# Kernel optimization log

Hardware: AMD Instinct MI355X
Metric: run time of the kernel (lower is better)

The kernel has to match this reference:

```python
import jax, jax.numpy as jnp
import numpy as np

N_GRIDS = 64          # n_grids
FEATS = 2             # feats_per_grid
DIM = 64              # feat_grid_dim (D=H=W)
N_PTS = 1 << 19       # query points per batch
N_NEURONS = 64        # tcnn FullyFusedMLP n_neurons


def setup_inputs() -> dict:
    key = jax.random.key(0)
    ks = jax.random.split(key, 8)
    x = jax.random.uniform(ks[0], (N_PTS, 3), jnp.float32, -1.0, 1.0)
    r = jax.random.normal(ks[1], (N_GRIDS, 4), jnp.float32)                      # quaternions
    s = 1.0 + 0.05 * jax.random.normal(ks[2], (N_GRIDS, 3), jnp.float32)         # scales ~1
    t = 0.1 * jax.random.normal(ks[3], (N_GRIDS, 3), jnp.float32)                # translations
    features = 0.1 * jax.random.normal(ks[4], (N_GRIDS, FEATS, DIM, DIM, DIM), jnp.float32)
    d_in = N_GRIDS * FEATS
    W0 = jax.random.normal(ks[5], (N_NEURONS, d_in), jnp.float32) / np.sqrt(d_in)
    W1 = jax.random.normal(ks[6], (N_NEURONS, N_NEURONS), jnp.float32) / np.sqrt(N_NEURONS)
    W2 = jax.random.normal(ks[7], (1, N_NEURONS), jnp.float32) / np.sqrt(N_NEURONS)
    return {"x": x, "r": r, "s": s, "t": t, "features": features,
            "W0": W0, "W1": W1, "W2": W2}


def quat_to_rot(q):
    # q: [G,4] (w,x,y,z); normalized rotation matrices [G,3,3]
    q = q / jnp.linalg.norm(q, axis=-1, keepdims=True)
    w, x, y, z = q[:, 0], q[:, 1], q[:, 2], q[:, 3]
    R = jnp.stack([
        1 - 2 * (y * y + z * z), 2 * (x * y - w * z),     2 * (x * z + w * y),
        2 * (x * y + w * z),     1 - 2 * (x * x + z * z), 2 * (y * z - w * x),
        2 * (x * z - w * y),     2 * (y * z + w * x),     1 - 2 * (x * x + y * y),
    ], axis=-1)
    return R.reshape(-1, 3, 3)


def trilinear_sample(features, pts):
    # features: [G,C,D,H,W]; pts: [G,N,3] in [-1,1], (x,y,z) -> (W,H,D) axes,
    # align_corners=True, zero padding (torch grid_sample semantics).
    G, C, D, H, W = features.shape
    gx = (pts[..., 0] + 1.0) * 0.5 * (W - 1)
    gy = (pts[..., 1] + 1.0) * 0.5 * (H - 1)
    gz = (pts[..., 2] + 1.0) * 0.5 * (D - 1)
    x0f, y0f, z0f = jnp.floor(gx), jnp.floor(gy), jnp.floor(gz)
    fx, fy, fz = gx - x0f, gy - y0f, gz - z0f
    x0, y0, z0 = x0f.astype(jnp.int32), y0f.astype(jnp.int32), z0f.astype(jnp.int32)
    x1, y1, z1 = x0 + 1, y0 + 1, z0 + 1
    feat_flat = features.reshape(G, C, D * H * W)

    def corner(xi, yi, zi, w):
        valid = ((xi >= 0) & (xi < W) & (yi >= 0) & (yi < H) & (zi >= 0) & (zi < D))
        xc = jnp.clip(xi, 0, W - 1)
        yc = jnp.clip(yi, 0, H - 1)
        zc = jnp.clip(zi, 0, D - 1)
        idx = (zc * H + yc) * W + xc                       # [G,N]
        v = jnp.take_along_axis(feat_flat, idx[:, None, :], axis=2)  # [G,C,N]
        return v * (w * valid)[:, None, :]

    out = (corner(x0, y0, z0, (1 - fx) * (1 - fy) * (1 - fz))
         + corner(x1, y0, z0, fx * (1 - fy) * (1 - fz))
         + corner(x0, y1, z0, (1 - fx) * fy * (1 - fz))
         + corner(x1, y1, z0, fx * fy * (1 - fz))
         + corner(x0, y0, z1, (1 - fx) * (1 - fy) * fz)
         + corner(x1, y0, z1, fx * (1 - fy) * fz)
         + corner(x0, y1, z1, (1 - fx) * fy * fz)
         + corner(x1, y1, z1, fx * fy * fz))
    return out  # [G,C,N]


def encode(x, r, s, t, features):
    R = quat_to_rot(r)                                     # [G,3,3]
    # per-grid affine: p' = (R p) * s + t  -> [G,N,3]
    tp = jnp.einsum('gij,nj->gni', R, x) * s[:, None, :] + t[:, None, :]
    sampled = trilinear_sample(features, tp)               # [G,C,N]
    N = x.shape[0]
    return jnp.transpose(sampled, (2, 0, 1)).reshape(N, -1)  # [N, G*C]


def reference(x, r, s, t, features, W0, W1, W2):
    feats = encode(x, r, s, t, features)                   # [N, 128]
    h = jax.nn.relu(feats @ W0.T)                          # [N, 64]
    h = jax.nn.relu(h @ W1.T)                              # [N, 64]
    return h @ W2.T                                        # [N, 1]
```

## Files before the change

### kernel.cpp

```cpp
#include <hip/hip_runtime.h>
#include <hip/hip_fp16.h>

#define NG    64
#define NC    2
#define DIMG  64
#define NPTS  (1u << 19)
#define NN    64
#define DIN   (NG * NC)
#define VOX   (DIMG * DIMG * DIMG)
#define CELLS 16
#define NCELL (CELLS * CELLS * CELLS)

typedef _Float16 f16;
typedef _Float16 f16x8 __attribute__((ext_vector_type(8)));
typedef float    f32x4 __attribute__((ext_vector_type(4)));

#define OFF_M      0
#define OFF_W0F    768
#define OFF_W1F    4864
#define OFF_HIST   6912
#define OFF_CNT    11008
#define OFF_SORT   15104
#define OFF_FEATP  2112256
#define WS_REQ_BYTES (((size_t)OFF_FEATP + 2ull * NG * VOX) * 4 + 64)

__device__ __forceinline__ f16x8 as_f16x8(uint4 u) {
    union { uint4 u; f16x8 h; } c; c.u = u; return c.h;
}
__device__ __forceinline__ float2 h2f(uint u) {
    union { uint u; __half2 h; } c; c.u = u; return __half22float2(c.h);
}

__global__ void prep_kernel(const float* __restrict__ r, const float* __restrict__ s,
                            const float* __restrict__ t, const float* __restrict__ W0,
                            const float* __restrict__ W1, float* __restrict__ ws) {
    int tid = blockIdx.x * blockDim.x + threadIdx.x;
    int nth = gridDim.x * blockDim.x;
    float* M  = ws + OFF_M;
    f16* W0f  = (f16*)(ws + OFF_W0F);
    f16* W1f  = (f16*)(ws + OFF_W1F);
    if (tid < NG) {
        float qw = r[tid*4+0], qx = r[tid*4+1], qy = r[tid*4+2], qz = r[tid*4+3];
        float inv = 1.0f / sqrtf(qw*qw + qx*qx + qy*qy + qz*qz);
        qw *= inv; qx *= inv; qy *= inv; qz *= inv;
        float R0 = 1.f - 2.f*(qy*qy + qz*qz), R1 = 2.f*(qx*qy - qw*qz), R2 = 2.f*(qx*qz + qw*qy);
        float R3 = 2.f*(qx*qy + qw*qz), R4 = 1.f - 2.f*(qx*qx + qz*qz), R5 = 2.f*(qy*qz - qw*qx);
        float R6 = 2.f*(qx*qz - qw*qy), R7 = 2.f*(qy*qz + qw*qx), R8 = 1.f - 2.f*(qx*qx + qy*qy);
        float s0 = s[tid*3+0], s1 = s[tid*3+1], s2 = s[tid*3+2];
        M[tid*12+ 0] = s0*R0; M[tid*12+ 1] = s0*R1; M[tid*12+ 2] = s0*R2; M[tid*12+ 3] = t[tid*3+0];
        M[tid*12+ 4] = s1*R3; M[tid*12+ 5] = s1*R4; M[tid*12+ 6] = s1*R5; M[tid*12+ 7] = t[tid*3+1];
        M[tid*12+ 8] = s2*R6; M[tid*12+ 9] = s2*R7; M[tid*12+10] = s2*R8; M[tid*12+11] = t[tid*3+2];
    }
    for (int idx = tid; idx < 4*4*64*8; idx += nth) {
        int tn = idx >> 11, kc = (idx >> 9) & 3, lane = (idx >> 3) & 63, j = idx & 7;
        int n = tn*16 + (lane & 15);
        int k = kc*32 + (lane >> 4)*8 + j;
        W0f[idx] = (f16)W0[n*DIN + k];
    }
    for (int idx = tid; idx < 4*2*64*8; idx += nth) {
        int tn = idx >> 10, kc2 = (idx >> 9) & 1, lane = (idx >> 3) & 63, j = idx & 7;
        int n = tn*16 + (lane & 15);
        int k = kc2*32 + (lane >> 4)*8 + j;
        W1f[idx] = (f16)W1[n*NN + k];
    }
}

__global__ __launch_bounds__(256) void repack_pairs(const float* __restrict__ feat,
                                                    uint4* __restrict__ featP4) {
    size_t i = (size_t)blockIdx.x * 256 + threadIdx.x;
    size_t g = i / (VOX/4), vq = i % (VOX/4);
    const float* b0 = feat + g * (size_t)(NC * VOX);
    const float* b1 = b0 + VOX;
    float4 a = ((const float4*)b0)[vq];
    float4 b = ((const float4*)b1)[vq];
    int vnext = (int)vq * 4 + 4; if (vnext > VOX - 1) vnext = VOX - 1;
    float a4 = b0[vnext], b4 = b1[vnext];
    __half2 h0 = __floats2half2_rn(a.x, b.x);
    __half2 h1 = __floats2half2_rn(a.y, b.y);
    __half2 h2 = __floats2half2_rn(a.z, b.z);
    __half2 h3 = __floats2half2_rn(a.w, b.w);
    __half2 h4 = __floats2half2_rn(a4, b4);
    union { uint4 u[2]; __half2 h[8]; } o;
    o.h[0] = h0; o.h[1] = h1;
    o.h[2] = h1; o.h[3] = h2;
    o.h[4] = h2; o.h[5] = h3;
    o.h[6] = h3; o.h[7] = h4;
    featP4[i*2 + 0] = o.u[0];
    featP4[i*2 + 1] = o.u[1];
}

__device__ __forceinline__ int cell_of(float px, float py, float pz) {
    int ix = (int)((px + 1.f) * (0.5f * CELLS)); ix = ix < 0 ? 0 : (ix > CELLS-1 ? CELLS-1 : ix);
    int iy = (int)((py + 1.f) * (0.5f * CELLS)); iy = iy < 0 ? 0 : (iy > CELLS-1 ? CELLS-1 : iy);
    int iz = (int)((pz + 1.f) * (0.5f * CELLS)); iz = iz < 0 ? 0 : (iz > CELLS-1 ? CELLS-1 : iz);
    return (iz * CELLS + iy) * CELLS + ix;
}

__global__ __launch_bounds__(256) void count_kernel(const float* __restrict__ xs,
                                                    unsigned* __restrict__ hist) {
    unsigned pt = blockIdx.x * blockDim.x + threadIdx.x;
    atomicAdd(&hist[cell_of(xs[pt*3+0], xs[pt*3+1], xs[pt*3+2])], 1u);
}

__global__ __launch_bounds__(256) void scan_kernel(const unsigned* __restrict__ hist,
                                                   unsigned* __restrict__ cnt) {
    __shared__ unsigned part[256];
    int t = threadIdx.x;
    unsigned base = t * (NCELL / 256);
    unsigned loc[NCELL / 256];
    unsigned sum = 0;
#pragma unroll
    for (int i = 0; i < NCELL / 256; ++i) { loc[i] = sum; sum += hist[base + i]; }
    part[t] = sum;
    __syncthreads();
    for (int off = 1; off < 256; off <<= 1) {
        unsigned v = (t >= off) ? part[t - off] : 0u;
        __syncthreads();
        part[t] += v;
        __syncthreads();
    }
    unsigned prev = (t == 0) ? 0u : part[t - 1];
#pragma unroll
    for (int i = 0; i < NCELL / 256; ++i) cnt[base + i] = prev + loc[i];
}

__global__ __launch_bounds__(256) void scatter_kernel(const float* __restrict__ xs,
                                                      unsigned* __restrict__ cnt,
                                                      float4* __restrict__ sorted) {
    unsigned pt = blockIdx.x * blockDim.x + threadIdx.x;
    float px = xs[pt*3+0], py = xs[pt*3+1], pz = xs[pt*3+2];
    unsigned pos = atomicAdd(&cnt[cell_of(px, py, pz)], 1u);
    sorted[pos] = make_float4(px, py, pz, __int_as_float((int)pt));
}

__global__ __launch_bounds__(256, 4) void amgsrn_fused(
        const float4* __restrict__ sorted, const uint2* __restrict__ featP,
        const float* __restrict__ ws, const float* __restrict__ W2,
        float* __restrict__ out) {
    __shared__ uint4 SH[2048];
    __shared__ float SOUT[256];
    const float* M = ws + OFF_M;
    const f16x8* W0f = (const f16x8*)(ws + OFF_W0F);
    const f16x8* W1f = (const f16x8*)(ws + OFF_W1F);

    int t = threadIdx.x;
    int lane = t & 63, w = t >> 6;
    int tmw = t >> 4, mrow = t & 15;

    float4 p4 = sorted[blockIdx.x * 256u + t];
    float px = p4.x, py = p4.y, pz = p4.z;
    int orig = __float_as_int(p4.w);

    f32x4 acc[4][4];
#pragma unroll
    for (int a = 0; a < 4; ++a)
#pragma unroll
        for (int b = 0; b < 4; ++b) acc[a][b] = (f32x4){0.f, 0.f, 0.f, 0.f};

    for (int kc = 0; kc < 4; ++kc) {
        uint4* buf = &SH[(kc & 1) * 1024];
#pragma unroll
        for (int c = 0; c < 4; ++c) {
            uint pk[4];
#pragma unroll
            for (int gi = 0; gi < 4; ++gi) {
                int g = kc * 16 + c * 4 + gi;
                const float* m = M + g * 12;
                float tx = m[0]*px + m[1]*py + m[2]*pz + m[3];
                float ty = m[4]*px + m[5]*py + m[6]*pz + m[7];
                float tz = m[8]*px + m[9]*py + m[10]*pz + m[11];
                float gx = (tx + 1.f) * (0.5f * (DIMG - 1));
                float gy = (ty + 1.f) * (0.5f * (DIMG - 1));
                float gz = (tz + 1.f) * (0.5f * (DIMG - 1));
                float f0 = 0.f, f1 = 0.f;
                if (gx > -1.f && gx < (float)DIMG && gy > -1.f && gy < (float)DIMG &&
                    gz > -1.f && gz < (float)DIMG) {
                    float x0f = floorf(gx), y0f = floorf(gy), z0f = floorf(gz);
                    float fx = gx - x0f, fy = gy - y0f, fz = gz - z0f;
                    int x0 = (int)x0f, y0 = (int)y0f, z0 = (int)z0f;
                    int x1 = x0 + 1, y1 = y0 + 1, z1 = z0 + 1;
                    float wx0 = (x0 >= 0)      ? (1.f - fx) : 0.f;
                    float wx1 = (x1 <= DIMG-1) ? fx         : 0.f;
                    float wy0 = (y0 >= 0)      ? (1.f - fy) : 0.f;
                    float wy1 = (y1 <= DIMG-1) ? fy         : 0.f;
                    float wz0 = (z0 >= 0)      ? (1.f - fz) : 0.f;
                    float wz1 = (z1 <= DIMG-1) ? fz         : 0.f;
                    int cx0 = max(x0, 0), cx1 = min(x1, DIMG-1);
                    int cy0 = max(y0, 0), cy1 = min(y1, DIMG-1);
                    int cz0 = max(z0, 0), cz1 = min(z1, DIMG-1);
                    bool adj = (cx1 == cx0 + 1);

                    const uint2* P = featP + (size_t)g * VOX;
                    int r00 = (cz0 * DIMG + cy0) * DIMG + cx0;
                    int r01 = (cz0 * DIMG + cy1) * DIMG + cx0;
                    int r10 = (cz1 * DIMG + cy0) * DIMG + cx0;
                    int r11 = (cz1 * DIMG + cy1) * DIMG + cx0;
                    uint2 e00 = P[r00], e01 = P[r01], e10 = P[r10], e11 = P[r11];
                    float2 l00 = h2f(e00.x), u00 = h2f(adj ? e00.y : e00.x);
                    float2 l01 = h2f(e01.x), u01 = h2f(adj ? e01.y : e01.x);
                    float2 l10 = h2f(e10.x), u10 = h2f(adj ? e10.y : e10.x);
                    float2 l11 = h2f(e11.x), u11 = h2f(adj ? e11.y : e11.x);

                    float w00 = wz0*wy0, w01 = wz0*wy1, w10 = wz1*wy0, w11 = wz1*wy1;
                    f0 = w00*(wx0*l00.x + wx1*u00.x) + w01*(wx0*l01.x + wx1*u01.x)
                       + w10*(wx0*l10.x + wx1*u10.x) + w11*(wx0*l11.x + wx1*u11.x);
                    f1 = w00*(wx0*l00.y + wx1*u00.y) + w01*(wx0*l01.y + wx1*u01.y)
                       + w10*(wx0*l10.y + wx1*u10.y) + w11*(wx0*l11.y + wx1*u11.y);
                }
                union { uint u; __half2 h; } pkc;
                pkc.h = __floats2half2_rn(f0, f1);
                pk[gi] = pkc.u;
            }
            buf[tmw * 64 + c * 16 + mrow] = make_uint4(pk[0], pk[1], pk[2], pk[3]);
        }
        __syncthreads();
#pragma unroll
        for (int im = 0; im < 4; ++im) {
            f16x8 af = as_f16x8(buf[(w * 4 + im) * 64 + lane]);
#pragma unroll
            for (int tn = 0; tn < 4; ++tn) {
                f16x8 bf = W0f[(tn * 4 + kc) * 64 + lane];
                acc[im][tn] = __builtin_amdgcn_mfma_f32_16x16x32_f16(af, bf, acc[im][tn], 0, 0, 0);
            }
        }
    }
    __syncthreads();

    f16* Hh = (f16*)SH;
#pragma unroll
    for (int im = 0; im < 4; ++im) {
        int tm = w * 4 + im;
#pragma unroll
        for (int tn = 0; tn < 4; ++tn) {
            int n = tn * 16 + (lane & 15);
            int kc2 = n >> 5, koct = (n >> 3) & 3, j = n & 7;
#pragma unroll
            for (int r = 0; r < 4; ++r) {
                int mloc = (lane >> 4) * 4 + r;
                Hh[tm * 1024 + kc2 * 512 + (koct * 16 + mloc) * 8 + j] =
                    (f16)fmaxf(acc[im][tn][r], 0.f);
            }
        }
    }
    __syncthreads();

    f32x4 acc2[4][4];
#pragma unroll
    for (int a = 0; a < 4; ++a)
#pragma unroll
        for (int b = 0; b < 4; ++b) acc2[a][b] = (f32x4){0.f, 0.f, 0.f, 0.f};
#pragma unroll
    for (int kc2 = 0; kc2 < 2; ++kc2) {
#pragma unroll
        for (int im = 0; im < 4; ++im) {
            f16x8 af = as_f16x8(SH[(w * 4 + im) * 128 + kc2 * 64 + lane]);
#pragma unroll
            for (int tn = 0; tn < 4; ++tn) {
                f16x8 bf = W1f[(tn * 2 + kc2) * 64 + lane];
                acc2[im][tn] = __builtin_amdgcn_mfma_f32_16x16x32_f16(af, bf, acc2[im][tn], 0, 0, 0);
            }
        }
    }

    float w2v[4];
#pragma unroll
    for (int tn = 0; tn < 4; ++tn) w2v[tn] = W2[tn * 16 + (lane & 15)];
    __syncthreads();
#pragma unroll
    for (int im = 0; im < 4; ++im) {
#pragma unroll
        for (int r = 0; r < 4; ++r) {
            float pp = 0.f;
#pragma unroll
            for (int tn = 0; tn < 4; ++tn) pp += fmaxf(acc2[im][tn][r], 0.f) * w2v[tn];
            pp += __shfl_xor(pp, 1);
            pp += __shfl_xor(pp, 2);
            pp += __shfl_xor(pp, 4);
            pp += __shfl_xor(pp, 8);
            if ((lane & 15) == 0)
                SOUT[w * 64 + im * 16 + (lane >> 4) * 4 + r] = pp;
        }
    }
    __syncthreads();
    out[orig] = SOUT[t];
}

__global__ __launch_bounds__(256) void amgsrn_fallback(
        const float* __restrict__ xs, const float* __restrict__ feat,
        const float* __restrict__ ws, const float* __restrict__ W0,
        const float* __restrict__ W1, const float* __restrict__ W2,
        float* __restrict__ out) {
    const float* M = ws + OFF_M;
    unsigned pt = blockIdx.x * blockDim.x + threadIdx.x;
    float px = xs[pt*3+0], py = xs[pt*3+1], pz = xs[pt*3+2];
    float h0[NN];
#pragma unroll
    for (int j = 0; j < NN; ++j) h0[j] = 0.f;
    for (int g = 0; g < NG; ++g) {
        const float* m = M + g * 12;
        float tx = m[0]*px + m[1]*py + m[2]*pz + m[3];
        float ty = m[4]*px + m[5]*py + m[6]*pz + m[7];
        float tz = m[8]*px + m[9]*py + m[10]*pz + m[11];
        float gx = (tx + 1.f) * (0.5f * (DIMG - 1));
        float gy = (ty + 1.f) * (0.5f * (DIMG - 1));
        float gz = (tz + 1.f) * (0.5f * (DIMG - 1));
        float f0 = 0.f, f1 = 0.f;
        if (gx > -1.f && gx < (float)DIMG && gy > -1.f && gy < (float)DIMG &&
            gz > -1.f && gz < (float)DIMG) {
            float x0f = floorf(gx), y0f = floorf(gy), z0f = floorf(gz);
            float fx = gx - x0f, fy = gy - y0f, fz = gz - z0f;
            int x0 = (int)x0f, y0 = (int)y0f, z0 = (int)z0f;
            int x1 = x0 + 1, y1 = y0 + 1, z1 = z0 + 1;
            float wx0 = (x0 >= 0)      ? (1.f - fx) : 0.f;
            float wx1 = (x1 <= DIMG-1) ? fx         : 0.f;
            float wy0 = (y0 >= 0)      ? (1.f - fy) : 0.f;
            float wy1 = (y1 <= DIMG-1) ? fy         : 0.f;
            float wz0 = (z0 >= 0)      ? (1.f - fz) : 0.f;
            float wz1 = (z1 <= DIMG-1) ? fz         : 0.f;
            int cx0 = max(x0, 0), cx1 = min(x1, DIMG-1);
            int cy0 = max(y0, 0), cy1 = min(y1, DIMG-1);
            int cz0 = max(z0, 0), cz1 = min(z1, DIMG-1);
            const float* b0 = feat + (size_t)g * (NC * VOX);
            const float* b1 = b0 + VOX;
            int r00 = (cz0 * DIMG + cy0) * DIMG;
            int r01 = (cz0 * DIMG + cy1) * DIMG;
            int r10 = (cz1 * DIMG + cy0) * DIMG;
            int r11 = (cz1 * DIMG + cy1) * DIMG;
            f0 = wz0*(wy0*(wx0*b0[r00+cx0] + wx1*b0[r00+cx1]) + wy1*(wx0*b0[r01+cx0] + wx1*b0[r01+cx1]))
               + wz1*(wy0*(wx0*b0[r10+cx0] + wx1*b0[r10+cx1]) + wy1*(wx0*b0[r11+cx0] + wx1*b0[r11+cx1]));
            f1 = wz0*(wy0*(wx0*b1[r00+cx0] + wx1*b1[r00+cx1]) + wy1*(wx0*b1[r01+cx0] + wx1*b1[r01+cx1]))
               + wz1*(wy0*(wx0*b1[r10+cx0] + wx1*b1[r10+cx1]) + wy1*(wx0*b1[r11+cx0] + wx1*b1[r11+cx1]));
        }
#pragma unroll
        for (int j = 0; j < NN; ++j) {
            h0[j] = fmaf(f0, W0[j*DIN + g*2 + 0], h0[j]);
            h0[j] = fmaf(f1, W0[j*DIN + g*2 + 1], h0[j]);
        }
    }
#pragma unroll
    for (int j = 0; j < NN; ++j) h0[j] = fmaxf(h0[j], 0.f);
    float outv = 0.f;
    for (int j = 0; j < NN; ++j) {
        float acc = 0.f;
#pragma unroll
        for (int k = 0; k < NN; ++k) acc = fmaf(h0[k], W1[j*NN + k], acc);
        outv = fmaf(fmaxf(acc, 0.f), W2[j], outv);
    }
    out[pt] = outv;
}

extern "C" void kernel_launch(void* const* d_in, const int* in_sizes, int n_in,
                              void* d_out, int out_size, void* d_ws, size_t ws_size,
                              hipStream_t stream) {
    const float* x    = (const float*)d_in[0];
    const float* r    = (const float*)d_in[1];
    const float* s    = (const float*)d_in[2];
    const float* t    = (const float*)d_in[3];
    const float* feat = (const float*)d_in[4];
    const float* W0   = (const float*)d_in[5];
    const float* W1   = (const float*)d_in[6];
    const float* W2   = (const float*)d_in[7];
    float* outp = (float*)d_out;
    float* ws   = (float*)d_ws;

    prep_kernel<<<64, 256, 0, stream>>>(r, s, t, W0, W1, ws);

    if (ws_size >= WS_REQ_BYTES) {
        unsigned* hist   = (unsigned*)(ws + OFF_HIST);
        unsigned* cnt    = (unsigned*)(ws + OFF_CNT);
        float4*   sorted = (float4*)(ws + OFF_SORT);
        uint4*    featP4 = (uint4*)(ws + OFF_FEATP);

        hipMemsetAsync(hist, 0, NCELL * sizeof(unsigned), stream);
        repack_pairs<<<(NG * VOX / 4) / 256, 256, 0, stream>>>(feat, featP4);
        count_kernel<<<NPTS / 256, 256, 0, stream>>>(x, hist);
        scan_kernel<<<1, 256, 0, stream>>>(hist, cnt);
        scatter_kernel<<<NPTS / 256, 256, 0, stream>>>(x, cnt, sorted);
        amgsrn_fused<<<NPTS / 256, 256, 0, stream>>>(sorted, (const uint2*)featP4, ws, W2, outp);
    } else {
        amgsrn_fallback<<<NPTS / 256, 256, 0, stream>>>(x, feat, ws, W0, W1, W2, outp);
    }
}
```

Before: 466.6 us.

## Merge prep into repack, fuse count with scan, use packed fp16 x-lerp

Folds the weight conversion, histogram zeroing and affine-matrix setup into the feature repack kernel. It also merges the histogram count and prefix scan into one kernel, where the last block to finish does the scan. This removes a memset and two kernel launches with their serialization gaps. The trilinear x-interpolation now runs in packed fp16 vector math before widening to fp32, which saves ALU work but lowers interpolation precision.

```diff
diff --git a/kernel.cpp b/kernel.cpp
--- a/kernel.cpp
+++ b/kernel.cpp
@@ -12,7 +12,9 @@
 #define NCELL (CELLS * CELLS * CELLS)
 
 typedef _Float16 f16;
+typedef _Float16 f16x2 __attribute__((ext_vector_type(2)));
 typedef _Float16 f16x8 __attribute__((ext_vector_type(8)));
+typedef float    f32x2 __attribute__((ext_vector_type(2)));
 typedef float    f32x4 __attribute__((ext_vector_type(4)));
 
 #define OFF_M      0
@@ -20,54 +22,58 @@
 #define OFF_W1F    4864
 #define OFF_HIST   6912
 #define OFF_CNT    11008
-#define OFF_SORT   15104
-#define OFF_FEATP  2112256
+#define OFF_DONE   15104
+#define OFF_SORT   15168
+#define OFF_FEATP  2112320
 #define WS_REQ_BYTES (((size_t)OFF_FEATP + 2ull * NG * VOX) * 4 + 64)
 
 __device__ __forceinline__ f16x8 as_f16x8(uint4 u) {
     union { uint4 u; f16x8 h; } c; c.u = u; return c.h;
 }
-__device__ __forceinline__ float2 h2f(uint u) {
-    union { uint u; __half2 h; } c; c.u = u; return __half22float2(c.h);
-}
-
-__global__ void prep_kernel(const float* __restrict__ r, const float* __restrict__ s,
-                            const float* __restrict__ t, const float* __restrict__ W0,
-                            const float* __restrict__ W1, float* __restrict__ ws) {
-    int tid = blockIdx.x * blockDim.x + threadIdx.x;
-    int nth = gridDim.x * blockDim.x;
-    float* M  = ws + OFF_M;
-    f16* W0f  = (f16*)(ws + OFF_W0F);
-    f16* W1f  = (f16*)(ws + OFF_W1F);
-    if (tid < NG) {
-        float qw = r[tid*4+0], qx = r[tid*4+1], qy = r[tid*4+2], qz = r[tid*4+3];
+__device__ __forceinline__ f16x2 uas_h2(uint u) {
+    union { uint u; f16x2 h; } c; c.u = u; return c.h;
+}
+
+__global__ __launch_bounds__(256) void prep_repack(
+        const float* __restrict__ r, const float* __restrict__ s,
+        const float* __restrict__ t, const float* __restrict__ W0,
+        const float* __restrict__ W1, const float* __restrict__ feat,
+        float* __restrict__ ws) {
+    unsigned i = blockIdx.x * 256u + threadIdx.x;
+
+    if (i < 8192) {
+        f16* W0f = (f16*)(ws + OFF_W0F);
+        int tn = i >> 11, kc = (i >> 9) & 3, lane = (i >> 3) & 63, j = i & 7;
+        int n = tn*16 + (lane & 15);
+        int k = kc*32 + (lane >> 4)*8 + j;
+        W0f[i] = (f16)W0[n*DIN + k];
+    } else if (i < 12288) {
+        f16* W1f = (f16*)(ws + OFF_W1F);
+        int idx = i - 8192;
+        int tn = idx >> 10, kc2 = (idx >> 9) & 1, lane = (idx >> 3) & 63, j = idx & 7;
+        int n = tn*16 + (lane & 15);
+        int k = kc2*32 + (lane >> 4)*8 + j;
+        W1f[idx] = (f16)W1[n*NN + k];
+    } else if (i < 16384) {
+        ((unsigned*)(ws + OFF_HIST))[i - 12288] = 0u;
+    } else if (i == 16384) {
+        ((unsigned*)(ws + OFF_DONE))[0] = 0u;
+    } else if (i >= 16448 && i < 16448 + NG) {
+        int g = i - 16448;
+        float* M = ws + OFF_M;
+        float qw = r[g*4+0], qx = r[g*4+1], qy = r[g*4+2], qz = r[g*4+3];
         float inv = 1.0f / sqrtf(qw*qw + qx*qx + qy*qy + qz*qz);
         qw *= inv; qx *= inv; qy *= inv; qz *= inv;
         float R0 = 1.f - 2.f*(qy*qy + qz*qz), R1 = 2.f*(qx*qy - qw*qz), R2 = 2.f*(qx*qz + qw*qy);
         float R3 = 2.f*(qx*qy + qw*qz), R4 = 1.f - 2.f*(qx*qx + qz*qz), R5 = 2.f*(qy*qz - qw*qx);
         float R6 = 2.f*(qx*qz - qw*qy), R7 = 2.f*(qy*qz + qw*qx), R8 = 1.f - 2.f*(qx*qx + qy*qy);
-        float s0 = s[tid*3+0], s1 = s[tid*3+1], s2 = s[tid*3+2];
-        M[tid*12+ 0] = s0*R0; M[tid*12+ 1] = s0*R1; M[tid*12+ 2] = s0*R2; M[tid*12+ 3] = t[tid*3+0];
-        M[tid*12+ 4] = s1*R3; M[tid*12+ 5] = s1*R4; M[tid*12+ 6] = s1*R5; M[tid*12+ 7] = t[tid*3+1];
-        M[tid*12+ 8] = s2*R6; M[tid*12+ 9] = s2*R7; M[tid*12+10] = s2*R8; M[tid*12+11] = t[tid*3+2];
-    }
-    for (int idx = tid; idx < 4*4*64*8; idx += nth) {
-        int tn = idx >> 11, kc = (idx >> 9) & 3, lane = (idx >> 3) & 63, j = idx & 7;
-        int n = tn*16 + (lane & 15);
-        int k = kc*32 + (lane >> 4)*8 + j;
-        W0f[idx] = (f16)W0[n*DIN + k];
-    }
-    for (int idx = tid; idx < 4*2*64*8; idx += nth) {
-        int tn = idx >> 10, kc2 = (idx >> 9) & 1, lane = (idx >> 3) & 63, j = idx & 7;
-        int n = tn*16 + (lane & 15);
-        int k = kc2*32 + (lane >> 4)*8 + j;
-        W1f[idx] = (f16)W1[n*NN + k];
-    }
-}
-
-__global__ __launch_bounds__(256) void repack_pairs(const float* __restrict__ feat,
-                                                    uint4* __restrict__ featP4) {
-    size_t i = (size_t)blockIdx.x * 256 + threadIdx.x;
+        float s0 = s[g*3+0], s1 = s[g*3+1], s2 = s[g*3+2];
+        M[g*12+ 0] = s0*R0; M[g*12+ 1] = s0*R1; M[g*12+ 2] = s0*R2; M[g*12+ 3] = t[g*3+0];
+        M[g*12+ 4] = s1*R3; M[g*12+ 5] = s1*R4; M[g*12+ 6] = s1*R5; M[g*12+ 7] = t[g*3+1];
+        M[g*12+ 8] = s2*R6; M[g*12+ 9] = s2*R7; M[g*12+10] = s2*R8; M[g*12+11] = t[g*3+2];
+    }
+
+    uint4* featP4 = (uint4*)(ws + OFF_FEATP);
     size_t g = i / (VOX/4), vq = i % (VOX/4);
     const float* b0 = feat + g * (size_t)(NC * VOX);
     const float* b1 = b0 + VOX;
@@ -85,8 +91,8 @@
     o.h[2] = h1; o.h[3] = h2;
     o.h[4] = h2; o.h[5] = h3;
     o.h[6] = h3; o.h[7] = h4;
-    featP4[i*2 + 0] = o.u[0];
-    featP4[i*2 + 1] = o.u[1];
+    featP4[(size_t)i*2 + 0] = o.u[0];
+    featP4[(size_t)i*2 + 1] = o.u[1];
 }
 
 __device__ __forceinline__ int cell_of(float px, float py, float pz) {
@@ -96,38 +102,48 @@
     return (iz * CELLS + iy) * CELLS + ix;
 }
 
-__global__ __launch_bounds__(256) void count_kernel(const float* __restrict__ xs,
-                                                    unsigned* __restrict__ hist) {
-    unsigned pt = blockIdx.x * blockDim.x + threadIdx.x;
+__global__ __launch_bounds__(256) void count_scan(const float* __restrict__ xs,
+                                                  unsigned* __restrict__ hist,
+                                                  unsigned* __restrict__ cnt,
+                                                  unsigned* __restrict__ done) {
+    unsigned pt = blockIdx.x * 256u + threadIdx.x;
     atomicAdd(&hist[cell_of(xs[pt*3+0], xs[pt*3+1], xs[pt*3+2])], 1u);
-}
-
-__global__ __launch_bounds__(256) void scan_kernel(const unsigned* __restrict__ hist,
-                                                   unsigned* __restrict__ cnt) {
-    __shared__ unsigned part[256];
-    int t = threadIdx.x;
-    unsigned base = t * (NCELL / 256);
-    unsigned loc[NCELL / 256];
-    unsigned sum = 0;
-#pragma unroll
-    for (int i = 0; i < NCELL / 256; ++i) { loc[i] = sum; sum += hist[base + i]; }
-    part[t] = sum;
-    __syncthreads();
-    for (int off = 1; off < 256; off <<= 1) {
-        unsigned v = (t >= off) ? part[t - off] : 0u;
+    __threadfence();
+    __syncthreads();
+    __shared__ unsigned isLast;
+    if (threadIdx.x == 0)
+        isLast = (atomicAdd(done, 1u) == gridDim.x - 1) ? 1u : 0u;
+    __syncthreads();
+    if (isLast) {
+        __threadfence();
+        __shared__ unsigned part[256];
+        int t = threadIdx.x;
+        unsigned base = t * (NCELL / 256);
+        unsigned loc[NCELL / 256];
+        unsigned sum = 0;
+#pragma unroll
+        for (int k = 0; k < NCELL / 256; ++k) {
+            loc[k] = sum;
+            sum += atomicAdd(&hist[base + k], 0u);
+        }
+        part[t] = sum;
         __syncthreads();
-        part[t] += v;
-        __syncthreads();
-    }
-    unsigned prev = (t == 0) ? 0u : part[t - 1];
-#pragma unroll
-    for (int i = 0; i < NCELL / 256; ++i) cnt[base + i] = prev + loc[i];
+        for (int off = 1; off < 256; off <<= 1) {
+            unsigned v = (t >= off) ? part[t - off] : 0u;
+            __syncthreads();
+            part[t] += v;
+            __syncthreads();
+        }
+        unsigned prev = (t == 0) ? 0u : part[t - 1];
+#pragma unroll
+        for (int k = 0; k < NCELL / 256; ++k) cnt[base + k] = prev + loc[k];
+    }
 }
 
 __global__ __launch_bounds__(256) void scatter_kernel(const float* __restrict__ xs,
                                                       unsigned* __restrict__ cnt,
                                                       float4* __restrict__ sorted) {
-    unsigned pt = blockIdx.x * blockDim.x + threadIdx.x;
+    unsigned pt = blockIdx.x * 256u + threadIdx.x;
     float px = xs[pt*3+0], py = xs[pt*3+1], pz = xs[pt*3+2];
     unsigned pos = atomicAdd(&cnt[cell_of(px, py, pz)], 1u);
     sorted[pos] = make_float4(px, py, pz, __int_as_float((int)pt));
@@ -172,7 +188,7 @@
                 float gx = (tx + 1.f) * (0.5f * (DIMG - 1));
                 float gy = (ty + 1.f) * (0.5f * (DIMG - 1));
                 float gz = (tz + 1.f) * (0.5f * (DIMG - 1));
-                float f0 = 0.f, f1 = 0.f;
+                f32x2 fv = (f32x2){0.f, 0.f};
                 if (gx > -1.f && gx < (float)DIMG && gy > -1.f && gy < (float)DIMG &&
                     gz > -1.f && gz < (float)DIMG) {
                     float x0f = floorf(gx), y0f = floorf(gy), z0f = floorf(gz);
@@ -196,19 +212,19 @@
                     int r10 = (cz1 * DIMG + cy0) * DIMG + cx0;
                     int r11 = (cz1 * DIMG + cy1) * DIMG + cx0;
                     uint2 e00 = P[r00], e01 = P[r01], e10 = P[r10], e11 = P[r11];
-                    float2 l00 = h2f(e00.x), u00 = h2f(adj ? e00.y : e00.x);
-                    float2 l01 = h2f(e01.x), u01 = h2f(adj ? e01.y : e01.x);
-                    float2 l10 = h2f(e10.x), u10 = h2f(adj ? e10.y : e10.x);
-                    float2 l11 = h2f(e11.x), u11 = h2f(adj ? e11.y : e11.x);
-
+                    f16 hwx0 = (f16)wx0, hwx1 = (f16)wx1;
+                    f16x2 rx00 = uas_h2(e00.x)*hwx0 + uas_h2(adj ? e00.y : e00.x)*hwx1;
+                    f16x2 rx01 = uas_h2(e01.x)*hwx0 + uas_h2(adj ? e01.y : e01.x)*hwx1;
+                    f16x2 rx10 = uas_h2(e10.x)*hwx0 + uas_h2(adj ? e10.y : e10.x)*hwx1;
+                    f16x2 rx11 = uas_h2(e11.x)*hwx0 + uas_h2(adj ? e11.y : e11.x)*hwx1;
                     float w00 = wz0*wy0, w01 = wz0*wy1, w10 = wz1*wy0, w11 = wz1*wy1;
-                    f0 = w00*(wx0*l00.x + wx1*u00.x) + w01*(wx0*l01.x + wx1*u01.x)
-                       + w10*(wx0*l10.x + wx1*u10.x) + w11*(wx0*l11.x + wx1*u11.x);
-                    f1 = w00*(wx0*l00.y + wx1*u00.y) + w01*(wx0*l01.y + wx1*u01.y)
-                       + w10*(wx0*l10.y + wx1*u10.y) + w11*(wx0*l11.y + wx1*u11.y);
+                    fv  = __builtin_convertvector(rx00, f32x2) * w00;
+                    fv += __builtin_convertvector(rx01, f32x2) * w01;
+                    fv += __builtin_convertvector(rx10, f32x2) * w10;
+                    fv += __builtin_convertvector(rx11, f32x2) * w11;
                 }
                 union { uint u; __half2 h; } pkc;
-                pkc.h = __floats2half2_rn(f0, f1);
+                pkc.h = __floats2half2_rn(fv.x, fv.y);
                 pk[gi] = pkc.u;
             }
             buf[tmw * 64 + c * 16 + mrow] = make_uint4(pk[0], pk[1], pk[2], pk[3]);
@@ -283,6 +299,23 @@
     }
     __syncthreads();
     out[orig] = SOUT[t];
+}
+
+__global__ void prep_M(const float* __restrict__ r, const float* __restrict__ s,
+                       const float* __restrict__ t, float* __restrict__ ws) {
+    int g = threadIdx.x;
+    if (g >= NG) return;
+    float* M = ws + OFF_M;
+    float qw = r[g*4+0], qx = r[g*4+1], qy = r[g*4+2], qz = r[g*4+3];
+    float inv = 1.0f / sqrtf(qw*qw + qx*qx + qy*qy + qz*qz);
+    qw *= inv; qx *= inv; qy *= inv; qz *= inv;
+    float R0 = 1.f - 2.f*(qy*qy + qz*qz), R1 = 2.f*(qx*qy - qw*qz), R2 = 2.f*(qx*qz + qw*qy);
+    float R3 = 2.f*(qx*qy + qw*qz), R4 = 1.f - 2.f*(qx*qx + qz*qz), R5 = 2.f*(qy*qz - qw*qx);
+    float R6 = 2.f*(qx*qz - qw*qy), R7 = 2.f*(qy*qz + qw*qx), R8 = 1.f - 2.f*(qx*qx + qy*qy);
+    float s0 = s[g*3+0], s1 = s[g*3+1], s2 = s[g*3+2];
+    M[g*12+ 0] = s0*R0; M[g*12+ 1] = s0*R1; M[g*12+ 2] = s0*R2; M[g*12+ 3] = t[g*3+0];
+    M[g*12+ 4] = s1*R3; M[g*12+ 5] = s1*R4; M[g*12+ 6] = s1*R5; M[g*12+ 7] = t[g*3+1];
+    M[g*12+ 8] = s2*R6; M[g*12+ 9] = s2*R7; M[g*12+10] = s2*R8; M[g*12+11] = t[g*3+2];
 }
 
 __global__ __launch_bounds__(256) void amgsrn_fallback(
@@ -363,21 +396,19 @@
     float* outp = (float*)d_out;
     float* ws   = (float*)d_ws;
 
-    prep_kernel<<<64, 256, 0, stream>>>(r, s, t, W0, W1, ws);
-
     if (ws_size >= WS_REQ_BYTES) {
         unsigned* hist   = (unsigned*)(ws + OFF_HIST);
         unsigned* cnt    = (unsigned*)(ws + OFF_CNT);
+        unsigned* done   = (unsigned*)(ws + OFF_DONE);
         float4*   sorted = (float4*)(ws + OFF_SORT);
-        uint4*    featP4 = (uint4*)(ws + OFF_FEATP);
-
-        hipMemsetAsync(hist, 0, NCELL * sizeof(unsigned), stream);
-        repack_pairs<<<(NG * VOX / 4) / 256, 256, 0, stream>>>(feat, featP4);
-        count_kernel<<<NPTS / 256, 256, 0, stream>>>(x, hist);
-        scan_kernel<<<1, 256, 0, stream>>>(hist, cnt);
+        uint2*    featP  = (uint2*)(ws + OFF_FEATP);
+
+        prep_repack<<<(NG * VOX / 4) / 256, 256, 0, stream>>>(r, s, t, W0, W1, feat, ws);
+        count_scan<<<NPTS / 256, 256, 0, stream>>>(x, hist, cnt, done);
         scatter_kernel<<<NPTS / 256, 256, 0, stream>>>(x, cnt, sorted);
-        amgsrn_fused<<<NPTS / 256, 256, 0, stream>>>(sorted, (const uint2*)featP4, ws, W2, outp);
+        amgsrn_fused<<<NPTS / 256, 256, 0, stream>>>(sorted, featP, ws, W2, outp);
     } else {
+        prep_M<<<1, 64, 0, stream>>>(r, s, t, ws);
         amgsrn_fallback<<<NPTS / 256, 256, 0, stream>>>(x, feat, ws, W0, W1, W2, outp);
     }
 }
```

New measurement: 564.4 us. +21.0%, slower.
